# Kernel optimization log

Measured on AMD Instinct MI355X. Metric: run time of the kernel, lower is better.

Reference implementation:

```python
import jax, jax.numpy as jnp
import numpy as np

B, L, D, H, NE, M = 4, 1024, 768, 12, 42, 8
OFFSET = 1
NEG = -1e9

def setup_inputs() -> dict:
    key = jax.random.key(0)
    k1, k2, k3, k4 = jax.random.split(key, 4)
    sequence_output = jax.random.normal(k1, (B, L, D), dtype=jnp.float32)
    attention = jax.random.uniform(k2, (B, H, L, L), dtype=jnp.float32)
    mention_idx = jax.random.randint(k3, (B, NE, M), 0, L - 2).astype(jnp.int32)
    mention_mask = jax.random.randint(k4, (B, NE, M), 0, 2).astype(jnp.int32)
    mention_mask = mention_mask.at[:, :, 0].set(1)  # every entity has >=1 mention
    return {"sequence_output": sequence_output, "attention": attention,
            "mention_idx": mention_idx, "mention_mask": mention_mask}

def reference(sequence_output, attention, mention_idx, mention_mask):
    b, l, d = sequence_output.shape
    h = attention.shape[1]
    idx = mention_idx + OFFSET                      # start + offset
    valid = (mention_mask > 0) & (idx < l)          # [B,NE,M], mirrors start+offset < c check
    idx = jnp.where(valid, idx, 0)

    # --- get_hrt: entity embedding = logsumexp over mentions, entity attn = mean over mentions ---
    flat = idx.reshape(b, -1)
    emb = jax.vmap(lambda s, i: s[i])(sequence_output, flat).reshape(b, NE, M, d)
    masked = jnp.where(valid[..., None], emb, NEG)
    ent_emb = jax.nn.logsumexp(masked, axis=2)      # [B,NE,D] (unused downstream, kept faithful)

    att = jax.vmap(lambda a, i: a[:, i])(attention, flat)        # [B,H,NE*M,L]
    att = att.reshape(b, h, NE, M, l)
    vmask = valid.astype(att.dtype)[:, None, :, :, None]         # [B,1,NE,M,1]
    cnt = jnp.maximum(valid.sum(axis=2), 1).astype(att.dtype)    # [B,NE]
    ent_att = (att * vmask).sum(axis=3) / cnt[:, None, :, None]  # [B,H,NE,L]

    # --- get_channel_map: ht_att = mean_h(h_att * t_att), row-normalize, contract with tokens ---
    ht_att = jnp.einsum('bhsl,bhtl->bstl', ent_att, ent_att) / h  # [B,NE,NE,L]
    ht_att = ht_att / (ht_att.sum(axis=-1, keepdims=True) + 1e-5)
    feature_map = jnp.einsum('bstl,bld->bstd', ht_att, sequence_output)  # [B,NE,NE,D]
    return feature_map
```

## Files before the change

### kernel.cpp

```cpp
#include <hip/hip_runtime.h>

#define B_    4
#define L_    1024
#define D_    768
#define H_    12
#define NE_   42
#define M_    8
#define NE2_  (NE_ * NE_)
#define MPAD_ 1792

typedef unsigned short u16;
typedef unsigned int   u32;

__device__ __forceinline__ u16 f2bf(float f) {
    union { float f; u32 u; } c; c.f = f;
    u32 u = c.u;
    u32 r = (u + 0x7FFFu + ((u >> 16) & 1u)) >> 16;
    return (u16)r;
}

__global__ __launch_bounds__(128) void ent_att_kernel(
    const float* __restrict__ att, const int* __restrict__ midx,
    const int* __restrict__ mmask, float* __restrict__ ent,
    float* __restrict__ D) {
    const int h = blockIdx.x, e = blockIdx.y, b = blockIdx.z;
    const int t  = threadIdx.x;

    if (h == 0 && e == 0) {
        for (int i = t; i < NE2_; i += 128) D[b * NE2_ + i] = 0.f;
    }

    const int l0 = t * 8;
    const int mb = (b * NE_ + e) * M_;
    const size_t abase = ((size_t)(b * H_ + h)) * L_ * L_;

    float acc[8] = {0.f,0.f,0.f,0.f,0.f,0.f,0.f,0.f};
    int cnt = 0;
    for (int m = 0; m < M_; ++m) {
        int  im = midx[mb + m] + 1;
        bool v  = (mmask[mb + m] > 0) && (im < L_);
        if (v) {
            ++cnt;
            const float* row = att + abase + (size_t)im * L_ + l0;
            float4 x0 = *(const float4*)(row);
            float4 x1 = *(const float4*)(row + 4);
            acc[0] += x0.x; acc[1] += x0.y; acc[2] += x0.z; acc[3] += x0.w;
            acc[4] += x1.x; acc[5] += x1.y; acc[6] += x1.z; acc[7] += x1.w;
        }
    }
    const float s = 1.0f / (float)(cnt < 1 ? 1 : cnt);
    float* o = ent + (((size_t)(b * H_ + h)) * NE_ + e) * L_ + l0;
    *(float4*)(o)     = make_float4(acc[0]*s, acc[1]*s, acc[2]*s, acc[3]*s);
    *(float4*)(o + 4) = make_float4(acc[4]*s, acc[5]*s, acc[6]*s, acc[7]*s);
}

__global__ __launch_bounds__(256) void transpose_kernel(
    const float* __restrict__ S, u16* __restrict__ T) {
    __shared__ u16 tile[32][33];
    const int b  = blockIdx.z;
    const int n0 = blockIdx.x * 32;
    const int k0 = blockIdx.y * 32;
    const int tx = threadIdx.x, ty = threadIdx.y;
    const float* Sb = S + (size_t)b * L_ * D_;
    u16*         Tb = T + (size_t)b * D_ * L_;
    #pragma unroll
    for (int i = 0; i < 4; ++i)
        tile[ty + i*8][tx] = f2bf(Sb[(size_t)(k0 + ty + i*8) * D_ + (n0 + tx)]);
    __syncthreads();
    #pragma unroll
    for (int i = 0; i < 4; ++i)
        Tb[(size_t)(n0 + ty + i*8) * L_ + (k0 + tx)] = tile[tx][ty + i*8];
}

#define LQ_    256
#define PAD3A  260

__global__ __launch_bounds__(256) void denom_kernel(
    const float* __restrict__ ent, float* __restrict__ D) {
    __shared__ float es[44 * PAD3A];
    const int lq = blockIdx.x, h = blockIdx.y, b = blockIdx.z;
    const int tid = threadIdx.x;
    const float* Eb = ent + ((size_t)(b * H_ + h) * NE_) * L_ + lq * LQ_;

    for (int i = tid; i < 44 * 64; i += 256) {
        int r = i >> 6, c = i & 63;
        float4 v = (r < NE_) ? *(const float4*)(Eb + (size_t)r * L_ + c * 4)
                             : make_float4(0.f, 0.f, 0.f, 0.f);
        *(float4*)&es[r * PAD3A + c * 4] = v;
    }
    __syncthreads();

    float* Db = D + b * NE2_;
    for (int item = tid; item < 242; item += 256) {
        const int tile = item >> 1, lh = item & 1;
        const int s0 = (tile / 11) * 4, t0 = (tile % 11) * 4;
        const float* ps = es + lh * 128;
        float a[4][4] = {};
        for (int l4 = 0; l4 < 32; ++l4) {
            float4 sv[4], tv[4];
            #pragma unroll
            for (int j = 0; j < 4; ++j) {
                sv[j] = *(const float4*)&ps[(s0 + j) * PAD3A + l4 * 4];
                tv[j] = *(const float4*)&ps[(t0 + j) * PAD3A + l4 * 4];
            }
            #pragma unroll
            for (int j = 0; j < 4; ++j)
                #pragma unroll
                for (int k = 0; k < 4; ++k)
                    a[j][k] += sv[j].x*tv[k].x + sv[j].y*tv[k].y
                             + sv[j].z*tv[k].z + sv[j].w*tv[k].w;
        }
        #pragma unroll
        for (int j = 0; j < 4; ++j)
            #pragma unroll
            for (int k = 0; k < 4; ++k) {
                int s = s0 + j, t = t0 + k;
                if (s < NE_ && t < NE_) atomicAdd(Db + s * NE_ + t, a[j][k]);
            }
    }
}

__global__ __launch_bounds__(256) void wbuild_kernel(
    const float* __restrict__ ent, const float* __restrict__ D,
    u16* __restrict__ W) {
    __shared__ float eb[H_ * NE_ * 16];
    const int lc = blockIdx.x, b = blockIdx.y;
    const int tid = threadIdx.x;
    const float* Eb = ent + (size_t)b * H_ * NE_ * L_ + lc * 16;

    for (int i = tid; i < H_ * NE_ * 4; i += 256) {
        int he = i >> 2, c4 = i & 3;
        *(float4*)&eb[he * 16 + c4 * 4] = *(const float4*)(Eb + (size_t)he * L_ + c4 * 4);
    }
    __syncthreads();

    const int lane = tid & 63, w = tid >> 6;
    const int lg = lane & 3, tg = lane >> 2;
    const float* Db = D + b * NE2_;
    u16* Wb = W + ((size_t)b * MPAD_) * L_ + lc * 16 + lg * 4;

    for (int s = w; s < NE_; s += 4) {
        float4 es[H_];
        #pragma unroll
        for (int h = 0; h < H_; ++h)
            es[h] = *(const float4*)&eb[(h * NE_ + s) * 16 + lg * 4];
        for (int t = tg; t < NE_; t += 16) {
            const float dv = Db[s * NE_ + t];
            float4 a = {0.f, 0.f, 0.f, 0.f};
            #pragma unroll
            for (int h = 0; h < H_; ++h) {
                float4 e2 = *(const float4*)&eb[(h * NE_ + t) * 16 + lg * 4];
                a.x += es[h].x * e2.x; a.y += es[h].y * e2.y;
                a.z += es[h].z * e2.z; a.w += es[h].w * e2.w;
            }
            const float inv = 1.0f / (dv + (float)H_ * 1e-5f);
            ushort4 o;
            o.x = f2bf(a.x * inv); o.y = f2bf(a.y * inv);
            o.z = f2bf(a.z * inv); o.w = f2bf(a.w * inv);
            *(ushort4*)(Wb + (size_t)(s * NE_ + t) * L_) = o;
        }
    }
    for (int i = tid; i < (MPAD_ - NE2_) * 16; i += 256) {
        int p = NE2_ + (i >> 4), l = i & 15;
        W[((size_t)b * MPAD_ + p) * L_ + lc * 16 + l] = 0;
    }
}

typedef __attribute__((ext_vector_type(8))) __bf16 bf16x8;
typedef __attribute__((ext_vector_type(4))) float  f32x4;

__global__ __launch_bounds__(256) void gemm_kernel(
    const u16* __restrict__ W, const u16* __restrict__ T, float* __restrict__ out) {
    __shared__ __align__(16) u16 As[128 * 32];
    __shared__ __align__(16) u16 Bs[64 * 32];
    const int b = blockIdx.z;
    const u16* Ab = W + (size_t)b * MPAD_ * L_ + (size_t)blockIdx.x * 128 * L_;
    const u16* Bb = T + (size_t)b * D_   * L_ + (size_t)blockIdx.y * 64  * L_;
    const int tid  = threadIdx.x;
    const int wave = tid >> 6, lane = tid & 63;
    const int wm = (wave & 1) * 64, wn = (wave >> 1) * 32;
    const int rm = lane & 15, kq = (lane >> 4) * 8;

    f32x4 acc[4][2] = {};

    for (int k0 = 0; k0 < L_; k0 += 32) {
        __syncthreads();
        #pragma unroll
        for (int i = 0; i < 2; ++i) {
            int c = i * 256 + tid;
            int row = c >> 2, ko = (c & 3) * 8;
            __builtin_amdgcn_global_load_lds(
                (const __attribute__((address_space(1))) void*)(Ab + (size_t)row * L_ + k0 + ko),
                (__attribute__((address_space(3))) void*)(&As[c * 8]), 16, 0, 0);
        }
        {
            int c = tid;
            int row = c >> 2, ko = (c & 3) * 8;
            __builtin_amdgcn_global_load_lds(
                (const __attribute__((address_space(1))) void*)(Bb + (size_t)row * L_ + k0 + ko),
                (__attribute__((address_space(3))) void*)(&Bs[c * 8]), 16, 0, 0);
        }
        __syncthreads();

        bf16x8 af[4], bfr[2];
        #pragma unroll
        for (int i = 0; i < 4; ++i)
            af[i]  = *(const bf16x8*)&As[(wm + i*16 + rm) * 32 + kq];
        #pragma unroll
        for (int j = 0; j < 2; ++j)
            bfr[j] = *(const bf16x8*)&Bs[(wn + j*16 + rm) * 32 + kq];
        #pragma unroll
        for (int i = 0; i < 4; ++i)
            #pragma unroll
            for (int j = 0; j < 2; ++j)
                acc[i][j] = __builtin_amdgcn_mfma_f32_16x16x32_bf16(
                                af[i], bfr[j], acc[i][j], 0, 0, 0);
    }

    const int row0 = blockIdx.x * 128 + wm;
    const int col0 = blockIdx.y * 64  + wn;
    const int cl = lane & 15, rq = (lane >> 4) * 4;
    float* Ob = out + (size_t)b * NE2_ * D_;
    #pragma unroll
    for (int i = 0; i < 4; ++i) {
        #pragma unroll
        for (int j = 0; j < 2; ++j) {
            const int col = col0 + j*16 + cl;
            #pragma unroll
            for (int r = 0; r < 4; ++r) {
                const int row = row0 + i*16 + rq + r;
                if (row < NE2_)
                    Ob[(size_t)row * D_ + col] = acc[i][j][r];
            }
        }
    }
}

#define ENT_BYTES (8257536)
#define W_BYTES   (14680064)
#define ST_BYTES  (6291456)

extern "C" void kernel_launch(void* const* d_in, const int* in_sizes, int n_in,
                              void* d_out, int out_size, void* d_ws, size_t ws_size,
                              hipStream_t stream) {
    const float* seq   = (const float*)d_in[0];
    const float* att   = (const float*)d_in[1];
    const int*   midx  = (const int*)d_in[2];
    const int*   mmask = (const int*)d_in[3];
    float* out = (float*)d_out;

    char* ws  = (char*)d_ws;
    float* ent = (float*)ws;
    u16*   W   = (u16*)(ws + ENT_BYTES);
    u16*   ST  = (u16*)(ws + ENT_BYTES + W_BYTES);
    float* Dd  = (float*)(ws + ENT_BYTES + W_BYTES + ST_BYTES);

    ent_att_kernel<<<dim3(H_, NE_, B_), 128, 0, stream>>>(att, midx, mmask, ent, Dd);
    transpose_kernel<<<dim3(D_/32, L_/32, B_), dim3(32, 8), 0, stream>>>(seq, ST);
    denom_kernel<<<dim3(4, H_, B_), 256, 0, stream>>>(ent, Dd);
    wbuild_kernel<<<dim3(64, B_), 256, 0, stream>>>(ent, Dd, W);
    gemm_kernel<<<dim3(MPAD_/128, D_/64, B_), 256, 0, stream>>>(W, ST, out);
}
```

Measured before the change: 343.3 us.

## Fuse entity-attention and transpose kernels; replace denom atomics with slotted partial reduction

The entity-attention averaging and the bf16 transpose of the sequence output now run in one kernel launch, with block ranges split between the two tasks so they can overlap. The denominator kernel writes per-block partial sums into 96 slots instead of using atomicAdd, and a new small kernel reduces those slots. This removes float atomic contention, removes the in-kernel zeroing of D, and makes the sum order deterministic. The cost is an extra launch and a partial-sum buffer. The ent-att blocks also change from 128 to 256 threads, each loading one float4.

```diff
diff --git a/kernel.cpp b/kernel.cpp
--- a/kernel.cpp
+++ b/kernel.cpp
@@ -19,64 +19,57 @@
     return (u16)r;
 }
 
-__global__ __launch_bounds__(128) void ent_att_kernel(
+__global__ __launch_bounds__(256) void entatt_transpose_kernel(
     const float* __restrict__ att, const int* __restrict__ midx,
-    const int* __restrict__ mmask, float* __restrict__ ent,
-    float* __restrict__ D) {
-    const int h = blockIdx.x, e = blockIdx.y, b = blockIdx.z;
-    const int t  = threadIdx.x;
-
-    if (h == 0 && e == 0) {
-        for (int i = t; i < NE2_; i += 128) D[b * NE2_ + i] = 0.f;
-    }
-
-    const int l0 = t * 8;
-    const int mb = (b * NE_ + e) * M_;
-    const size_t abase = ((size_t)(b * H_ + h)) * L_ * L_;
-
-    float acc[8] = {0.f,0.f,0.f,0.f,0.f,0.f,0.f,0.f};
-    int cnt = 0;
-    for (int m = 0; m < M_; ++m) {
-        int  im = midx[mb + m] + 1;
-        bool v  = (mmask[mb + m] > 0) && (im < L_);
-        if (v) {
-            ++cnt;
-            const float* row = att + abase + (size_t)im * L_ + l0;
-            float4 x0 = *(const float4*)(row);
-            float4 x1 = *(const float4*)(row + 4);
-            acc[0] += x0.x; acc[1] += x0.y; acc[2] += x0.z; acc[3] += x0.w;
-            acc[4] += x1.x; acc[5] += x1.y; acc[6] += x1.z; acc[7] += x1.w;
-        }
-    }
-    const float s = 1.0f / (float)(cnt < 1 ? 1 : cnt);
-    float* o = ent + (((size_t)(b * H_ + h)) * NE_ + e) * L_ + l0;
-    *(float4*)(o)     = make_float4(acc[0]*s, acc[1]*s, acc[2]*s, acc[3]*s);
-    *(float4*)(o + 4) = make_float4(acc[4]*s, acc[5]*s, acc[6]*s, acc[7]*s);
-}
-
-__global__ __launch_bounds__(256) void transpose_kernel(
-    const float* __restrict__ S, u16* __restrict__ T) {
+    const int* __restrict__ mmask, const float* __restrict__ S,
+    float* __restrict__ ent, u16* __restrict__ T) {
     __shared__ u16 tile[32][33];
-    const int b  = blockIdx.z;
-    const int n0 = blockIdx.x * 32;
-    const int k0 = blockIdx.y * 32;
-    const int tx = threadIdx.x, ty = threadIdx.y;
-    const float* Sb = S + (size_t)b * L_ * D_;
-    u16*         Tb = T + (size_t)b * D_ * L_;
-    #pragma unroll
-    for (int i = 0; i < 4; ++i)
-        tile[ty + i*8][tx] = f2bf(Sb[(size_t)(k0 + ty + i*8) * D_ + (n0 + tx)]);
-    __syncthreads();
-    #pragma unroll
-    for (int i = 0; i < 4; ++i)
-        Tb[(size_t)(n0 + ty + i*8) * L_ + (k0 + tx)] = tile[tx][ty + i*8];
+    const int x = blockIdx.x, b = blockIdx.z;
+    const int tid = threadIdx.x;
+
+    if (x < H_ * NE_) {
+        const int h = x % H_, e = x / H_;
+        const int l0 = tid * 4;
+        const int mb = (b * NE_ + e) * M_;
+        const size_t abase = ((size_t)(b * H_ + h)) * L_ * L_;
+
+        float4 acc = {0.f, 0.f, 0.f, 0.f};
+        int cnt = 0;
+        for (int m = 0; m < M_; ++m) {
+            int  im = midx[mb + m] + 1;
+            bool v  = (mmask[mb + m] > 0) && (im < L_);
+            if (v) {
+                ++cnt;
+                float4 xv = *(const float4*)(att + abase + (size_t)im * L_ + l0);
+                acc.x += xv.x; acc.y += xv.y; acc.z += xv.z; acc.w += xv.w;
+            }
+        }
+        const float s = 1.0f / (float)(cnt < 1 ? 1 : cnt);
+        float* o = ent + (((size_t)(b * H_ + h)) * NE_ + e) * L_ + l0;
+        *(float4*)o = make_float4(acc.x*s, acc.y*s, acc.z*s, acc.w*s);
+    } else {
+        const int y  = x - H_ * NE_;
+        const int n0 = (y % (D_/32)) * 32;
+        const int k0 = (y / (D_/32)) * 32;
+        const int tx = tid & 31, ty = tid >> 5;
+        const float* Sb = S + (size_t)b * L_ * D_;
+        u16*         Tb = T + (size_t)b * D_ * L_;
+        #pragma unroll
+        for (int i = 0; i < 4; ++i)
+            tile[ty + i*8][tx] = f2bf(Sb[(size_t)(k0 + ty + i*8) * D_ + (n0 + tx)]);
+        __syncthreads();
+        #pragma unroll
+        for (int i = 0; i < 4; ++i)
+            Tb[(size_t)(n0 + ty + i*8) * L_ + (k0 + tx)] = tile[tx][ty + i*8];
+    }
 }
 
 #define LQ_    256
 #define PAD3A  260
+#define NSLOT  96
 
 __global__ __launch_bounds__(256) void denom_kernel(
-    const float* __restrict__ ent, float* __restrict__ D) {
+    const float* __restrict__ ent, float* __restrict__ Dpart) {
     __shared__ float es[44 * PAD3A];
     const int lq = blockIdx.x, h = blockIdx.y, b = blockIdx.z;
     const int tid = threadIdx.x;
@@ -90,10 +83,11 @@
     }
     __syncthreads();
 
-    float* Db = D + b * NE2_;
+    float* Dp = Dpart + (size_t)b * NE2_ * NSLOT;
     for (int item = tid; item < 242; item += 256) {
         const int tile = item >> 1, lh = item & 1;
         const int s0 = (tile / 11) * 4, t0 = (tile % 11) * 4;
+        const int slot = (h * 4 + lq) * 2 + lh;
         const float* ps = es + lh * 128;
         float a[4][4] = {};
         for (int l4 = 0; l4 < 32; ++l4) {
@@ -115,9 +109,24 @@
             #pragma unroll
             for (int k = 0; k < 4; ++k) {
                 int s = s0 + j, t = t0 + k;
-                if (s < NE_ && t < NE_) atomicAdd(Db + s * NE_ + t, a[j][k]);
-            }
-    }
+                if (s < NE_ && t < NE_)
+                    Dp[(size_t)(s * NE_ + t) * NSLOT + slot] = a[j][k];
+            }
+    }
+}
+
+__global__ __launch_bounds__(256) void reduce_d_kernel(
+    const float* __restrict__ Dpart, float* __restrict__ D) {
+    const int i = blockIdx.x * 256 + threadIdx.x;
+    if (i >= B_ * NE2_) return;
+    const float4* p = (const float4*)(Dpart + (size_t)i * NSLOT);
+    float4 s4 = {0.f, 0.f, 0.f, 0.f};
+    #pragma unroll
+    for (int j = 0; j < NSLOT / 4; ++j) {
+        float4 v = p[j];
+        s4.x += v.x; s4.y += v.y; s4.z += v.z; s4.w += v.w;
+    }
+    D[i] = s4.x + s4.y + s4.z + s4.w;
 }
 
 __global__ __launch_bounds__(256) void wbuild_kernel(
@@ -239,6 +248,7 @@
 #define ENT_BYTES (8257536)
 #define W_BYTES   (14680064)
 #define ST_BYTES  (6291456)
+#define D_BYTES   (28224)
 
 extern "C" void kernel_launch(void* const* d_in, const int* in_sizes, int n_in,
                               void* d_out, int out_size, void* d_ws, size_t ws_size,
@@ -250,14 +260,16 @@
     float* out = (float*)d_out;
 
     char* ws  = (char*)d_ws;
-    float* ent = (float*)ws;
-    u16*   W   = (u16*)(ws + ENT_BYTES);
-    u16*   ST  = (u16*)(ws + ENT_BYTES + W_BYTES);
-    float* Dd  = (float*)(ws + ENT_BYTES + W_BYTES + ST_BYTES);
-
-    ent_att_kernel<<<dim3(H_, NE_, B_), 128, 0, stream>>>(att, midx, mmask, ent, Dd);
-    transpose_kernel<<<dim3(D_/32, L_/32, B_), dim3(32, 8), 0, stream>>>(seq, ST);
-    denom_kernel<<<dim3(4, H_, B_), 256, 0, stream>>>(ent, Dd);
+    float* ent   = (float*)ws;
+    u16*   W     = (u16*)(ws + ENT_BYTES);
+    u16*   ST    = (u16*)(ws + ENT_BYTES + W_BYTES);
+    float* Dd    = (float*)(ws + ENT_BYTES + W_BYTES + ST_BYTES);
+    float* Dpart = (float*)(ws + ENT_BYTES + W_BYTES + ST_BYTES + D_BYTES);
+
+    entatt_transpose_kernel<<<dim3(H_*NE_ + (D_/32)*(L_/32), 1, B_), 256, 0, stream>>>(
+        att, midx, mmask, seq, ent, ST);
+    denom_kernel<<<dim3(4, H_, B_), 256, 0, stream>>>(ent, Dpart);
+    reduce_d_kernel<<<(B_ * NE2_ + 255) / 256, 256, 0, stream>>>(Dpart, Dd);
     wbuild_kernel<<<dim3(64, B_), 256, 0, stream>>>(ent, Dd, W);
     gemm_kernel<<<dim3(MPAD_/128, D_/64, B_), 256, 0, stream>>>(W, ST, out);
 }
```

Result: faster. 317.6 us (-7.5%).
